# Performance work log

Measured on AMD Instinct MI355X. Metric: run time of the kernel, lower is better.

The kernel has to match this reference:

```python
import jax, jax.numpy as jnp
import numpy as np

N_EMBD = 768
N_EXPERTS = 8
TOP_K = 2
D_FF = 4 * N_EMBD


def setup_inputs() -> dict:
    key = jax.random.key(0)
    k1, k2, k3, k4 = jax.random.split(key, 4)
    x = jax.random.normal(k1, (2, 2048, N_EMBD), dtype=jnp.float32)
    gate_w = jax.random.normal(k2, (N_EMBD, N_EXPERTS), dtype=jnp.float32) * (1.0 / np.sqrt(N_EMBD))
    w_fc = jax.random.normal(k3, (N_EXPERTS, N_EMBD, D_FF), dtype=jnp.float32) * (1.0 / np.sqrt(N_EMBD))
    w_proj = jax.random.normal(k4, (N_EXPERTS, D_FF, N_EMBD), dtype=jnp.float32) * (1.0 / np.sqrt(D_FF))
    return {"x": x, "gate_w": gate_w, "w_fc": w_fc, "w_proj": w_proj}


def reference(x, gate_w, w_fc, w_proj):
    B, S, D = x.shape
    E = w_fc.shape[0]
    xt = x.reshape(-1, D)                    # [T, D]
    T = xt.shape[0]
    scores = xt @ gate_w                      # [T, E]
    expert_weights, expert_indices = jax.lax.top_k(scores, TOP_K)  # [T, K]
    expert_weights = jax.nn.softmax(expert_weights, axis=-1)
    # per-token combine weight for each expert (0 if expert not selected)
    comb = jnp.zeros((T, E), dtype=xt.dtype)
    comb = comb.at[jnp.arange(T)[:, None], expert_indices].add(expert_weights)  # [T, E]
    out = jnp.zeros_like(xt)
    for e in range(E):  # fixed small loop over experts
        h = jax.nn.gelu(xt @ w_fc[e], approximate=False)  # torch nn.GELU default = exact erf
        y_e = h @ w_proj[e]                               # [T, D]
        out = out + comb[:, e:e + 1] * y_e
    return out.reshape(B, S, D)
```

## Files before the change

### kernel.cpp

```cpp
#include <hip/hip_runtime.h>
#include <hip/hip_bf16.h>
#include <math.h>

#define T_TOK 4096
#define D_EMB 768
#define DFF   3072
#define N_EXP 8
#define MAXT2 40
#define CNTS  16

typedef __attribute__((ext_vector_type(8))) short bf16x8;
typedef __attribute__((ext_vector_type(4))) float f32x4;

typedef __attribute__((address_space(3))) unsigned int lds_u32_t;
typedef __attribute__((address_space(1))) unsigned int glob_u32_t;

__device__ __forceinline__ void gload16(const void* g, void* l) {
  __builtin_amdgcn_global_load_lds((const glob_u32_t*)g, (lds_u32_t*)l, 16, 0, 0);
}

__device__ __forceinline__ short f2bf(float f) {
  union { __hip_bfloat16 b; short s; } u;
  u.b = __float2bfloat16(f);
  return u.s;
}

__global__ void zero_init_kernel(float4* __restrict__ out4, int n4, int* __restrict__ cnt) {
  int i = blockIdx.x * blockDim.x + threadIdx.x;
  if (i < N_EXP * CNTS) cnt[i] = 0;
  float4 z; z.x = z.y = z.z = z.w = 0.f;
  for (int j = i; j < n4; j += gridDim.x * blockDim.x) out4[j] = z;
}

__global__ void cast_x_kernel(const float4* __restrict__ in, short4* __restrict__ outp, int n4) {
  int i = blockIdx.x * blockDim.x + threadIdx.x;
  if (i >= n4) return;
  float4 v = in[i];
  short4 o;
  o.x = f2bf(v.x); o.y = f2bf(v.y); o.z = f2bf(v.z); o.w = f2bf(v.w);
  outp[i] = o;
}

__global__ void transpose_cast_kernel(const float* __restrict__ in, short* __restrict__ outp,
                                      int R, int C) {
  __shared__ float tile[64][65];
  int e = blockIdx.z;
  int c0 = blockIdx.x * 64, r0 = blockIdx.y * 64;
  const float* src = in + (size_t)e * R * C;
  short* dst = outp + (size_t)e * R * C;
  int tid = threadIdx.x;
#pragma unroll
  for (int it = 0; it < 4; ++it) {
    int idx = tid + it * 256;
    int r = idx >> 4;
    int c4 = idx & 15;
    float4 v = *(const float4*)&src[(size_t)(r0 + r) * C + c0 + c4 * 4];
    tile[r][c4 * 4 + 0] = v.x; tile[r][c4 * 4 + 1] = v.y;
    tile[r][c4 * 4 + 2] = v.z; tile[r][c4 * 4 + 3] = v.w;
  }
  __syncthreads();
#pragma unroll
  for (int it = 0; it < 4; ++it) {
    int idx = tid + it * 256;
    int c = idx >> 4;
    int rr = idx & 15;
    short4 o;
    o.x = f2bf(tile[rr * 4 + 0][c]);
    o.y = f2bf(tile[rr * 4 + 1][c]);
    o.z = f2bf(tile[rr * 4 + 2][c]);
    o.w = f2bf(tile[rr * 4 + 3][c]);
    *(short4*)&dst[(size_t)(c0 + c) * R + r0 + rr * 4] = o;
  }
}

__global__ __launch_bounds__(256)
void gate_kernel(const float* __restrict__ x, const float* __restrict__ gw,
                 int* __restrict__ cnt, int* __restrict__ tok,
                 float* __restrict__ wgt) {
  __shared__ int lcnt[N_EXP];
  __shared__ int gbase[N_EXP];
  __shared__ int le[32];
  __shared__ float lw[32];
  __shared__ int lpos[32];
  int tid = threadIdx.x, lane = tid & 63, wid = tid >> 6;
  if (tid < N_EXP) lcnt[tid] = 0;
  __syncthreads();

#pragma unroll
  for (int i = 0; i < 4; i++) {
    int t = blockIdx.x * 16 + wid * 4 + i;
    float s[N_EXP];
#pragma unroll
    for (int e = 0; e < N_EXP; e++) s[e] = 0.f;
#pragma unroll
    for (int dd = 0; dd < D_EMB / 64; dd++) {
      int d = dd * 64 + lane;
      float xv = x[(size_t)t * D_EMB + d];
#pragma unroll
      for (int e = 0; e < N_EXP; e++) s[e] += xv * gw[d * N_EXP + e];
    }
#pragma unroll
    for (int e = 0; e < N_EXP; e++) {
#pragma unroll
      for (int off = 32; off > 0; off >>= 1) s[e] += __shfl_xor(s[e], off, 64);
    }
    if (lane == 0) {
      int e0 = 0;
#pragma unroll
      for (int e = 1; e < N_EXP; e++) if (s[e] > s[e0]) e0 = e;
      int e1 = -1;
#pragma unroll
      for (int e = 0; e < N_EXP; e++) {
        if (e == e0) continue;
        if (e1 < 0 || s[e] > s[e1]) e1 = e;
      }
      float p1 = __expf(s[e1] - s[e0]);
      float inv = 1.f / (1.f + p1);
      int idx = (wid * 4 + i) * 2;
      le[idx] = e0; lw[idx] = inv;           lpos[idx] = atomicAdd(&lcnt[e0], 1);
      le[idx + 1] = e1; lw[idx + 1] = p1 * inv; lpos[idx + 1] = atomicAdd(&lcnt[e1], 1);
    }
  }
  __syncthreads();
  if (tid < N_EXP) gbase[tid] = atomicAdd(&cnt[tid * CNTS], lcnt[tid]);
  __syncthreads();
  if (tid < 32) {
    int e = le[tid];
    int t = blockIdx.x * 16 + (tid >> 1);
    int p = gbase[e] + lpos[tid];
    tok[e * T_TOK + p] = t;
    wgt[e * T_TOK + p] = lw[tid];
  }
}

__global__ void plan_kernel(const int* __restrict__ cnt, int* __restrict__ offs,
                            int* __restrict__ tile_e, int* __restrict__ tile_rt,
                            int* __restrict__ ntiles) {
  if (threadIdx.x != 0 || blockIdx.x != 0) return;
  int o = 0, nt = 0;
  for (int e = 0; e < N_EXP; e++) {
    offs[e] = o;
    int tc = (cnt[e * CNTS] + 255) >> 8;
    for (int i = 0; i < tc; i++) { tile_e[nt] = e; tile_rt[nt] = i; nt++; }
    o += cnt[e * CNTS];
  }
  *ntiles = nt;
}

template<int KDIM, int NDIM, int SPLITK, int EPI>
__global__ __launch_bounds__(1024, 4)
void moe_gemm(const short* __restrict__ A, const short* __restrict__ Bw,
              const int* __restrict__ tok, const float* __restrict__ wgt,
              const int* __restrict__ cnt, const int* __restrict__ offs,
              const int* __restrict__ tile_e, const int* __restrict__ tile_rt,
              const int* __restrict__ ntiles,
              short* __restrict__ hout, float* __restrict__ fout) {
  const int COLT = NDIM / 256;
  const int KS = KDIM / SPLITK;
  const int NKT = KS / 32;
  static_assert(NKT >= 2, "need at least 2 k-steps");

  int nwg = gridDim.x;
  int cpx = nwg >> 3;
  int logical = (blockIdx.x & 7) * cpx + (blockIdx.x >> 3);
  int ct = logical % COLT;
  int tile = (logical / COLT) % MAXT2;
  int sk = logical / (COLT * MAXT2);
  if (tile >= *ntiles) return;
  int e = tile_e[tile], rt = tile_rt[tile];
  int ne = cnt[e * CNTS];
  int base = offs[e];

  __shared__ __align__(16) short As[2][256 * 32];
  __shared__ __align__(16) short Bs[2][256 * 32];

  int tid = threadIdx.x;
  int lane = tid & 63;
  int wid = tid >> 6;

  const short* aptr;
  const short* bptr;
  int lofs;
  {
    int row = tid >> 2, p = tid & 3;
    int q = p ^ ((row ^ (row >> 2)) & 3);
    int r = rt * 256 + row;
    if (r >= ne) r = ne - 1;
    size_t ga = (EPI == 0) ? (size_t)tok[e * T_TOK + r] : (size_t)(base + r);
    aptr = A + ga * KDIM + sk * KS + q * 8;
    bptr = Bw + ((size_t)e * NDIM + ct * 256 + row) * KDIM + sk * KS + q * 8;
    lofs = tid * 8;
  }

  int wr = (wid >> 2) * 64, wc = (wid & 3) * 64;
  int cb = lane >> 4;

  int offa[4], offb[4];
#pragma unroll
  for (int m = 0; m < 4; m++) {
    int row = wr + m * 16 + (lane & 15);
    offa[m] = row * 32 + (cb ^ ((row ^ (row >> 2)) & 3)) * 8;
  }
#pragma unroll
  for (int n = 0; n < 4; n++) {
    int row = wc + n * 16 + (lane & 15);
    offb[n] = row * 32 + (cb ^ ((row ^ (row >> 2)) & 3)) * 8;
  }

  f32x4 acc[4][4];
#pragma unroll
  for (int m = 0; m < 4; m++)
#pragma unroll
    for (int n = 0; n < 4; n++) acc[m][n] = (f32x4){0.f, 0.f, 0.f, 0.f};

  gload16(aptr, &As[0][lofs]);
  gload16(bptr, &Bs[0][lofs]);
  __syncthreads();

  int cur = 0;
  for (int kt = 0; kt < NKT; ++kt) {
    if (kt + 1 < NKT) {
      int k0 = (kt + 1) * 32;
      gload16(aptr + k0, &As[cur ^ 1][lofs]);
      gload16(bptr + k0, &Bs[cur ^ 1][lofs]);
    }
    bf16x8 af[4], bv[4];
#pragma unroll
    for (int m = 0; m < 4; m++)
      af[m] = *(const bf16x8*)&As[cur][offa[m]];
#pragma unroll
    for (int n = 0; n < 4; n++)
      bv[n] = *(const bf16x8*)&Bs[cur][offb[n]];
#pragma unroll
    for (int m = 0; m < 4; m++)
#pragma unroll
      for (int n = 0; n < 4; n++)
        acc[m][n] = __builtin_amdgcn_mfma_f32_16x16x32_bf16(af[m], bv[n], acc[m][n], 0, 0, 0);
    __syncthreads();
    cur ^= 1;
  }

  int colbase = ct * 256 + wc;
#pragma unroll
  for (int m = 0; m < 4; m++) {
#pragma unroll
    for (int j = 0; j < 4; j++) {
      int rloc = rt * 256 + wr + m * 16 + ((lane >> 4) << 2) + j;
      if (rloc < ne) {
        if (EPI == 0) {
          size_t hrow = (size_t)(base + rloc) * NDIM;
#pragma unroll
          for (int n = 0; n < 4; n++) {
            float v = acc[m][n][j];
            float g = 0.5f * v * (1.0f + erff(v * 0.70710678118f));
            hout[hrow + colbase + n * 16 + (lane & 15)] = f2bf(g);
          }
        } else {
          int t = tok[e * T_TOK + rloc];
          float w = wgt[e * T_TOK + rloc];
          float* orow = fout + (size_t)t * NDIM + colbase + (lane & 15);
#pragma unroll
          for (int n = 0; n < 4; n++)
            atomicAdd(orow + n * 16, w * acc[m][n][j]);
        }
      }
    }
  }
}

extern "C" void kernel_launch(void* const* d_in, const int* in_sizes, int n_in,
                              void* d_out, int out_size, void* d_ws, size_t ws_size,
                              hipStream_t stream) {
  const float* x   = (const float*)d_in[0];
  const float* gw  = (const float*)d_in[1];
  const float* wfc = (const float*)d_in[2];
  const float* wpj = (const float*)d_in[3];
  float* out = (float*)d_out;

  char* ws = (char*)d_ws;
  const size_t SZ_XB = (size_t)T_TOK * D_EMB * 2;
  const size_t SZ_W  = (size_t)N_EXP * D_EMB * DFF * 2;
  const size_t SZ_H  = (size_t)2 * T_TOK * DFF * 2;
  short* xb   = (short*)(ws);
  short* wfcT = (short*)(ws + SZ_XB);
  short* wpjT = (short*)(ws + SZ_XB + SZ_W);
  short* h    = (short*)(ws + SZ_XB + 2 * SZ_W);
  char* p2    = ws + SZ_XB + 2 * SZ_W + SZ_H;
  int*   tok  = (int*)(p2);
  float* wgt  = (float*)(p2 + (size_t)N_EXP * T_TOK * 4);
  char* p3    = p2 + (size_t)N_EXP * T_TOK * 8;
  int*   cnt     = (int*)(p3);
  int*   offs    = (int*)(p3 + 1024);
  int*   tile_e  = (int*)(p3 + 1024 + 64);
  int*   tile_rt = (int*)(p3 + 1024 + 64 + 512);
  int*   ntiles  = (int*)(p3 + 1024 + 64 + 1024);

  int n4 = out_size / 4;
  zero_init_kernel<<<2048, 256, 0, stream>>>((float4*)out, n4, cnt);
  cast_x_kernel<<<(T_TOK * D_EMB / 4 + 255) / 256, 256, 0, stream>>>(
      (const float4*)x, (short4*)xb, T_TOK * D_EMB / 4);
  transpose_cast_kernel<<<dim3(DFF / 64, D_EMB / 64, N_EXP), 256, 0, stream>>>(wfc, wfcT, D_EMB, DFF);
  transpose_cast_kernel<<<dim3(D_EMB / 64, DFF / 64, N_EXP), 256, 0, stream>>>(wpj, wpjT, DFF, D_EMB);
  gate_kernel<<<T_TOK / 16, 256, 0, stream>>>(x, gw, cnt, tok, wgt);
  plan_kernel<<<1, 1, 0, stream>>>(cnt, offs, tile_e, tile_rt, ntiles);
  moe_gemm<D_EMB, DFF, 1, 0><<<MAXT2 * (DFF / 256), 1024, 0, stream>>>(
      xb, wfcT, tok, wgt, cnt, offs, tile_e, tile_rt, ntiles, h, nullptr);
  moe_gemm<DFF, D_EMB, 2, 1><<<2 * MAXT2 * (D_EMB / 256), 1024, 0, stream>>>(
      h, wpjT, tok, wgt, cnt, offs, tile_e, tile_rt, ntiles, nullptr, out);
}
```

Measured before the change: 244.7 us.

## Restructure MoE GEMM into 256x128 tiles with 3-slot LDS pipeline and K=64 steps

The grouped expert GEMM moves from 1024-thread 256x256 tiles with a double-buffered K=32 loop to 512-thread 256x128 tiles. The new loop uses K=64 steps and a triple-buffered LDS rotation, with explicit vmcnt waits, split barriers and raised wave priority around the MFMA blocks. The LDS swizzle is changed to an 8-way XOR layout for the wider K rows. The aim is to hide global-to-LDS latency better, cut barrier overhead per FLOP and put more workgroups in flight. In exchange it uses more LDS per block (about 144KB) and doubles the grid size.

New measurement: 238.2 us. -2.7%, faster.

```diff
diff --git a/kernel.cpp b/kernel.cpp
--- a/kernel.cpp
+++ b/kernel.cpp
@@ -148,17 +148,17 @@
 }
 
 template<int KDIM, int NDIM, int SPLITK, int EPI>
-__global__ __launch_bounds__(1024, 4)
+__global__ __launch_bounds__(512, 2)
 void moe_gemm(const short* __restrict__ A, const short* __restrict__ Bw,
               const int* __restrict__ tok, const float* __restrict__ wgt,
               const int* __restrict__ cnt, const int* __restrict__ offs,
               const int* __restrict__ tile_e, const int* __restrict__ tile_rt,
               const int* __restrict__ ntiles,
               short* __restrict__ hout, float* __restrict__ fout) {
-  const int COLT = NDIM / 256;
+  const int COLT = NDIM / 128;
   const int KS = KDIM / SPLITK;
-  const int NKT = KS / 32;
-  static_assert(NKT >= 2, "need at least 2 k-steps");
+  const int NT = KS / 64;
+  static_assert(NT % 3 == 0 && NT >= 6, "3-slot rotation needs NT%3==0");
 
   int nwg = gridDim.x;
   int cpx = nwg >> 3;
@@ -171,40 +171,57 @@
   int ne = cnt[e * CNTS];
   int base = offs[e];
 
-  __shared__ __align__(16) short As[2][256 * 32];
-  __shared__ __align__(16) short Bs[2][256 * 32];
+  __shared__ __align__(16) short LDS[3 * 24576];
+  const int SL0 = 0, SL1 = 24576, SL2 = 49152;
 
   int tid = threadIdx.x;
   int lane = tid & 63;
   int wid = tid >> 6;
 
-  const short* aptr;
-  const short* bptr;
-  int lofs;
-  {
-    int row = tid >> 2, p = tid & 3;
-    int q = p ^ ((row ^ (row >> 2)) & 3);
-    int r = rt * 256 + row;
-    if (r >= ne) r = ne - 1;
-    size_t ga = (EPI == 0) ? (size_t)tok[e * T_TOK + r] : (size_t)(base + r);
-    aptr = A + ga * KDIM + sk * KS + q * 8;
-    bptr = Bw + ((size_t)e * NDIM + ct * 256 + row) * KDIM + sk * KS + q * 8;
-    lofs = tid * 8;
-  }
-
-  int wr = (wid >> 2) * 64, wc = (wid & 3) * 64;
+  const short* gp00; const short* gp01; const short* gp02;
+  const short* gp10; const short* gp11; const short* gp12;
+  int lo00, lo01, lo02, lo10, lo11, lo12;
+#define MKSEG(SEG, GP, LO) do {                                              \
+    int s_ = (SEG);                                                          \
+    if (s_ < 2048) {                                                         \
+      int row_ = s_ >> 3, p_ = s_ & 7;                                       \
+      int q_ = p_ ^ (row_ & 7);                                              \
+      int r_ = rt * 256 + row_; if (r_ >= ne) r_ = ne - 1;                   \
+      size_t ga_ = (EPI == 0) ? (size_t)tok[e * T_TOK + r_] : (size_t)(base + r_); \
+      GP = A + ga_ * KDIM + sk * KS + q_ * 8;                                \
+      LO = s_ * 8;                                                           \
+    } else {                                                                 \
+      int t_ = s_ - 2048;                                                    \
+      int row_ = t_ >> 3, p_ = t_ & 7;                                       \
+      int q_ = p_ ^ (row_ & 7);                                              \
+      GP = Bw + ((size_t)e * NDIM + ct * 128 + row_) * KDIM + sk * KS + q_ * 8; \
+      LO = 16384 + t_ * 8;                                                   \
+    }                                                                        \
+  } while (0)
+  MKSEG(tid,        gp00, lo00);
+  MKSEG(tid + 512,  gp01, lo01);
+  MKSEG(tid + 1024, gp02, lo02);
+  MKSEG(tid + 1536, gp10, lo10);
+  MKSEG(tid + 2048, gp11, lo11);
+  MKSEG(tid + 2560, gp12, lo12);
+#undef MKSEG
+
+  int wr = (wid >> 1) * 64;
+  int wc = (wid & 1) * 64;
   int cb = lane >> 4;
 
-  int offa[4], offb[4];
+  int offA0[4], offA1[4], offB0[4], offB1[4];
 #pragma unroll
   for (int m = 0; m < 4; m++) {
     int row = wr + m * 16 + (lane & 15);
-    offa[m] = row * 32 + (cb ^ ((row ^ (row >> 2)) & 3)) * 8;
+    offA0[m] = row * 64 + ((cb ^ (row & 7)) * 8);
+    offA1[m] = row * 64 + (((cb + 4) ^ (row & 7)) * 8);
   }
 #pragma unroll
   for (int n = 0; n < 4; n++) {
     int row = wc + n * 16 + (lane & 15);
-    offb[n] = row * 32 + (cb ^ ((row ^ (row >> 2)) & 3)) * 8;
+    offB0[n] = row * 64 + ((cb ^ (row & 7)) * 8);
+    offB1[n] = row * 64 + (((cb + 4) ^ (row & 7)) * 8);
   }
 
   f32x4 acc[4][4];
@@ -213,34 +230,63 @@
 #pragma unroll
     for (int n = 0; n < 4; n++) acc[m][n] = (f32x4){0.f, 0.f, 0.f, 0.f};
 
-  gload16(aptr, &As[0][lofs]);
-  gload16(bptr, &Bs[0][lofs]);
-  __syncthreads();
-
-  int cur = 0;
-  for (int kt = 0; kt < NKT; ++kt) {
-    if (kt + 1 < NKT) {
-      int k0 = (kt + 1) * 32;
-      gload16(aptr + k0, &As[cur ^ 1][lofs]);
-      gload16(bptr + k0, &Bs[cur ^ 1][lofs]);
-    }
-    bf16x8 af[4], bv[4];
-#pragma unroll
-    for (int m = 0; m < 4; m++)
-      af[m] = *(const bf16x8*)&As[cur][offa[m]];
-#pragma unroll
-    for (int n = 0; n < 4; n++)
-      bv[n] = *(const bf16x8*)&Bs[cur][offb[n]];
-#pragma unroll
-    for (int m = 0; m < 4; m++)
-#pragma unroll
-      for (int n = 0; n < 4; n++)
-        acc[m][n] = __builtin_amdgcn_mfma_f32_16x16x32_bf16(af[m], bv[n], acc[m][n], 0, 0, 0);
-    __syncthreads();
-    cur ^= 1;
-  }
-
-  int colbase = ct * 256 + wc;
+#define STAGE0(SST, KOFF) do {                       \
+    gload16(gp00 + (KOFF), &LDS[(SST) + lo00]);      \
+    gload16(gp01 + (KOFF), &LDS[(SST) + lo01]);      \
+    gload16(gp02 + (KOFF), &LDS[(SST) + lo02]); } while (0)
+#define STAGE1(SST, KOFF) do {                       \
+    gload16(gp10 + (KOFF), &LDS[(SST) + lo10]);      \
+    gload16(gp11 + (KOFF), &LDS[(SST) + lo11]);      \
+    gload16(gp12 + (KOFF), &LDS[(SST) + lo12]); } while (0)
+
+#define PH(SRD, OA, OB, SST, DOST, WHICH, KOFF, VM) do {                     \
+    bf16x8 af_[4], bv_[4];                                                   \
+    _Pragma("unroll") for (int m_ = 0; m_ < 4; ++m_)                         \
+      af_[m_] = *(const bf16x8*)&LDS[(SRD) + OA[m_]];                        \
+    _Pragma("unroll") for (int n_ = 0; n_ < 4; ++n_)                         \
+      bv_[n_] = *(const bf16x8*)&LDS[(SRD) + OB[n_]];                        \
+    if (DOST) { if ((WHICH) == 0) STAGE0((SST), (KOFF)); else STAGE1((SST), (KOFF)); } \
+    if ((VM) == 6) asm volatile("s_waitcnt vmcnt(6)" ::: "memory");          \
+    else if ((VM) == 0) asm volatile("s_waitcnt vmcnt(0)" ::: "memory");     \
+    __builtin_amdgcn_s_barrier();                                            \
+    __builtin_amdgcn_s_setprio(1);                                           \
+    _Pragma("unroll") for (int m_ = 0; m_ < 4; ++m_)                         \
+      _Pragma("unroll") for (int n_ = 0; n_ < 4; ++n_)                       \
+        acc[m_][n_] = __builtin_amdgcn_mfma_f32_16x16x32_bf16(               \
+            af_[m_], bv_[n_], acc[m_][n_], 0, 0, 0);                         \
+    __builtin_amdgcn_s_setprio(0);                                           \
+    __builtin_amdgcn_s_barrier();                                            \
+  } while (0)
+
+#define TILE(SRD, SST, DOST, KOFF, VMB)                                      \
+    PH((SRD), offA0, offB0X, (SST), (DOST), 0, (KOFF), -1);                  \
+    PH((SRD), offA1, offB1X, (SST), (DOST), 1, (KOFF), (VMB))
+  int offB0X[4], offB1X[4];
+#pragma unroll
+  for (int n = 0; n < 4; n++) { offB0X[n] = 16384 + offB0[n]; offB1X[n] = 16384 + offB1[n]; }
+
+  STAGE0(SL0, 0);  STAGE1(SL0, 0);
+  STAGE0(SL1, 64); STAGE1(SL1, 64);
+  asm volatile("s_waitcnt vmcnt(6)" ::: "memory");
+  __builtin_amdgcn_s_barrier();
+
+#pragma unroll 1
+  for (int g = 0; g < NT / 3 - 1; ++g) {
+    int k2 = (3 * g + 2) * 64, k3 = (3 * g + 3) * 64, k4 = (3 * g + 4) * 64;
+    TILE(SL0, SL2, 1, k2, 6);
+    TILE(SL1, SL0, 1, k3, 6);
+    TILE(SL2, SL1, 1, k4, 6);
+  }
+  TILE(SL0, SL2, 1, (NT - 1) * 64, 6);
+  TILE(SL1, SL0, 0, 0, 0);
+  TILE(SL2, SL1, 0, 0, -1);
+
+#undef TILE
+#undef PH
+#undef STAGE0
+#undef STAGE1
+
+  int colbase = ct * 128 + wc;
 #pragma unroll
   for (int m = 0; m < 4; m++) {
 #pragma unroll
@@ -303,8 +349,8 @@
   transpose_cast_kernel<<<dim3(D_EMB / 64, DFF / 64, N_EXP), 256, 0, stream>>>(wpj, wpjT, DFF, D_EMB);
   gate_kernel<<<T_TOK / 16, 256, 0, stream>>>(x, gw, cnt, tok, wgt);
   plan_kernel<<<1, 1, 0, stream>>>(cnt, offs, tile_e, tile_rt, ntiles);
-  moe_gemm<D_EMB, DFF, 1, 0><<<MAXT2 * (DFF / 256), 1024, 0, stream>>>(
+  moe_gemm<D_EMB, DFF, 1, 0><<<MAXT2 * (DFF / 128), 512, 0, stream>>>(
       xb, wfcT, tok, wgt, cnt, offs, tile_e, tile_rt, ntiles, h, nullptr);
-  moe_gemm<DFF, D_EMB, 2, 1><<<2 * MAXT2 * (D_EMB / 256), 1024, 0, stream>>>(
+  moe_gemm<DFF, D_EMB, 2, 1><<<2 * MAXT2 * (D_EMB / 128), 512, 0, stream>>>(
       h, wpjT, tok, wgt, cnt, offs, tile_e, tile_rt, ntiles, nullptr, out);
 }
```
